# Performance work log

Measured on AMD Instinct MI355X. Metric: run time of the kernel, lower is better.

The kernel has to match this reference:

```python
import jax, jax.numpy as jnp
import numpy as np


def setup_inputs() -> dict:
    key = jax.random.key(0)
    k1, k2, k3 = jax.random.split(key, 3)
    B, H, S, D = 2, 16, 2048, 128
    q = jax.random.normal(k1, (B, H, S, D), dtype=jnp.float32)
    k = jax.random.normal(k2, (B, H, S, D), dtype=jnp.float32)
    v = jax.random.normal(k3, (B, H, S, D), dtype=jnp.float32)
    mask = jnp.ones((1, 1, S, S), dtype=bool)  # broadcastable; mask==0 -> -inf
    scale = jnp.array(1.0, dtype=jnp.float32)  # learnable scalar nn.Parameter
    return {"q": q, "k": k, "v": v, "mask": mask, "scale": scale}


def reference(q, k, v, mask, scale):
    # scores = (q @ k^T) * scale  -> [B,H,S,S]
    scores = jnp.einsum("bhsd,bhtd->bhst", q, k) * scale
    scores = jnp.where(mask, scores, -jnp.inf)
    attn = jax.nn.softmax(scores, axis=-1)
    out = jnp.einsum("bhst,bhtd->bhsd", attn, v)
    return out
```

## Files before the change

### kernel.cpp

```cpp
#include <hip/hip_runtime.h>
#include <hip/hip_bf16.h>
#include <math.h>
#include <stdint.h>

#define Bn 2
#define Hn 16
#define Sn 2048
#define Dn 128
#define KVBLK 64
#define NITER (Sn / KVBLK)
#define QBLK_WG 128
#define QT (Sn / QBLK_WG)
#define NWG (Bn * Hn * QT)
#define LOG2E 1.44269504088896340736f
#define RESCALE_THR 8.0f

typedef _Float16 f16x8 __attribute__((ext_vector_type(8)));
typedef _Float16 f16x4 __attribute__((ext_vector_type(4)));
typedef float f32x16 __attribute__((ext_vector_type(16)));
typedef int i32x4 __attribute__((ext_vector_type(4)));

__device__ __forceinline__ void swap32(int& a, int& b) {
    asm("v_permlane32_swap_b32 %0, %1" : "+v"(a), "+v"(b));
}

__global__ __launch_bounds__(256, 2)
void attn_fwd(const float* __restrict__ qp, const float* __restrict__ kp,
              const float* __restrict__ vp, const float* __restrict__ scale_p,
              float* __restrict__ op) {
    __shared__ _Float16 lds_k[KVBLK * Dn];
    __shared__ _Float16 lds_vt[Dn * KVBLK];

    const int tid  = threadIdx.x;
    const int wave = tid >> 6;
    const int lane = tid & 63;
    const int l31  = lane & 31;
    const int h    = lane >> 5;

    const int bid = blockIdx.x;
    const int wg  = (bid & 7) * (NWG / 8) + (bid >> 3);
    const int bh  = wg / QT;
    const int qt  = wg % QT;
    const int q0w = qt * QBLK_WG + wave * 32;

    const float lam = scale_p[0] * LOG2E;
    const size_t base = (size_t)bh * Sn * Dn;
    const float* qg = qp + base;
    const float* kg = kp + base;
    const float* vg = vp + base;

    f16x8 qf[8];
    {
        const float* qrow = qg + (size_t)(q0w + l31) * Dn + h * 8;
#pragma unroll
        for (int c = 0; c < 8; ++c) {
            float4 x = *(const float4*)(qrow + c * 16);
            float4 y = *(const float4*)(qrow + c * 16 + 4);
            f16x8 t;
            t[0] = (_Float16)(x.x * lam); t[1] = (_Float16)(x.y * lam);
            t[2] = (_Float16)(x.z * lam); t[3] = (_Float16)(x.w * lam);
            t[4] = (_Float16)(y.x * lam); t[5] = (_Float16)(y.y * lam);
            t[6] = (_Float16)(y.z * lam); t[7] = (_Float16)(y.w * lam);
            qf[c] = t;
        }
    }

    float4 kreg[8];
    float  vreg[32];
    const int vd  = tid & 127;
    const int vkb = (tid >> 7) * 32;

    auto load_tiles = [&](int it) {
        const int kv0 = it * KVBLK;
#pragma unroll
        for (int p = 0; p < 8; ++p) {
            const int idx = p * 256 + tid;
            kreg[p] = *(const float4*)(kg + (size_t)(kv0 + (idx >> 5)) * Dn + ((idx & 31) << 2));
        }
        const float* col = vg + (size_t)(kv0 + vkb) * Dn + vd;
#pragma unroll
        for (int j = 0; j < 32; ++j) vreg[j] = col[(size_t)j * Dn];
    };

    auto store_tiles = [&]() {
#pragma unroll
        for (int p = 0; p < 8; ++p) {
            const int idx = p * 256 + tid;
            const int kv = idx >> 5, d4 = (idx & 31) << 2;
            f16x4 w = { (_Float16)kreg[p].x, (_Float16)kreg[p].y,
                        (_Float16)kreg[p].z, (_Float16)kreg[p].w };
            const int byte = (kv * 256 + d4 * 2) ^ ((kv & 15) << 4);
            *(f16x4*)((char*)lds_k + byte) = w;
        }
#pragma unroll
        for (int w8 = 0; w8 < 4; ++w8) {
            f16x8 t;
#pragma unroll
            for (int e = 0; e < 8; ++e) t[e] = (_Float16)vreg[8 * w8 + e];
            const int byte = (vd * 128 + (vkb + 8 * w8) * 2) ^ ((vd & 7) << 4);
            *(f16x8*)((char*)lds_vt + byte) = t;
        }
    };

    f32x16 acc[4];
#pragma unroll
    for (int dt = 0; dt < 4; ++dt)
#pragma unroll
        for (int r = 0; r < 16; ++r) acc[dt][r] = 0.f;
    float m_run = -INFINITY, l_run = 0.f;

    const int swzk = (l31 & 15) << 4;
    const int swzv = (l31 & 7) << 4;

    load_tiles(0);
    for (int it = 0; it < NITER; ++it) {
        __syncthreads();
        store_tiles();
        __syncthreads();
        if (it + 1 < NITER) load_tiles(it + 1);

        f32x16 st[2];
#pragma unroll
        for (int s = 0; s < 2; ++s)
#pragma unroll
            for (int r = 0; r < 16; ++r) st[s][r] = 0.f;
#pragma unroll
        for (int s = 0; s < 2; ++s) {
            const char* kbase = (const char*)lds_k + (32 * s + l31) * 256;
#pragma unroll
            for (int c = 0; c < 8; ++c) {
                f16x8 kf = *(const f16x8*)(kbase + ((c * 32 + h * 16) ^ swzk));
                st[s] = __builtin_amdgcn_mfma_f32_32x32x16_f16(kf, qf[c], st[s], 0, 0, 0);
            }
        }

        float pmax = st[0][0];
#pragma unroll
        for (int r = 1; r < 16; ++r) pmax = fmaxf(pmax, st[0][r]);
#pragma unroll
        for (int r = 0; r < 16; ++r) pmax = fmaxf(pmax, st[1][r]);
        const float rowmax = fmaxf(pmax, __shfl_xor(pmax, 32, 64));

        if (!__all(rowmax <= m_run + RESCALE_THR)) {
            const float mnew = fmaxf(m_run, rowmax);
            const float corr = exp2f(m_run - mnew);
            m_run = mnew;
            l_run *= corr;
#pragma unroll
            for (int dt = 0; dt < 4; ++dt)
#pragma unroll
                for (int r = 0; r < 16; ++r) acc[dt][r] *= corr;
        }

        float rs = 0.f;
#pragma unroll
        for (int s = 0; s < 2; ++s)
#pragma unroll
            for (int r = 0; r < 16; ++r) {
                const float pv = exp2f(st[s][r] - m_run);
                st[s][r] = pv;
                rs += pv;
            }
        l_run += rs + __shfl_xor(rs, 32, 64);

        int pk[2][4][2];
#pragma unroll
        for (int s = 0; s < 2; ++s)
#pragma unroll
            for (int c4 = 0; c4 < 4; ++c4) {
                pk[s][c4][0] = __builtin_bit_cast(int,
                    __builtin_amdgcn_cvt_pkrtz(st[s][4 * c4 + 0], st[s][4 * c4 + 1]));
                pk[s][c4][1] = __builtin_bit_cast(int,
                    __builtin_amdgcn_cvt_pkrtz(st[s][4 * c4 + 2], st[s][4 * c4 + 3]));
            }

#pragma unroll
        for (int ks = 0; ks < 4; ++ks) {
            const int s = ks >> 1, c0 = (ks & 1) * 2;
            int a0 = pk[s][c0][0],     a1 = pk[s][c0][1];
            int b0 = pk[s][c0 + 1][0], b1 = pk[s][c0 + 1][1];
            swap32(a0, b0);
            swap32(a1, b1);
            i32x4 bi = { a0, a1, b0, b1 };
            f16x8 bf = __builtin_bit_cast(f16x8, bi);
            const int voff = (ks * 32 + h * 16) ^ swzv;
#pragma unroll
            for (int dt = 0; dt < 4; ++dt) {
                f16x8 vf = *(const f16x8*)((const char*)lds_vt + (32 * dt + l31) * 128 + voff);
                acc[dt] = __builtin_amdgcn_mfma_f32_32x32x16_f16(vf, bf, acc[dt], 0, 0, 0);
            }
        }
    }

    const float inv = 1.0f / l_run;
    float* orow = op + base + (size_t)(q0w + l31) * Dn;
#pragma unroll
    for (int dt = 0; dt < 4; ++dt)
#pragma unroll
        for (int rg = 0; rg < 4; ++rg) {
            float4 w = { acc[dt][4 * rg + 0] * inv, acc[dt][4 * rg + 1] * inv,
                         acc[dt][4 * rg + 2] * inv, acc[dt][4 * rg + 3] * inv };
            *(float4*)(orow + 32 * dt + 8 * rg + 4 * h) = w;
        }
}

extern "C" void kernel_launch(void* const* d_in, const int* in_sizes, int n_in,
                              void* d_out, int out_size, void* d_ws, size_t ws_size,
                              hipStream_t stream) {
    const float* q = (const float*)d_in[0];
    const float* k = (const float*)d_in[1];
    const float* v = (const float*)d_in[2];
    const float* scale = (const float*)d_in[4];
    float* out = (float*)d_out;
    attn_fwd<<<dim3(NWG), dim3(256), 0, stream>>>(q, k, v, scale, out);
}
```

Measured before the change: 115.0 us.

## Pre-convert K/V to swizzled fp16 tiles and pipeline attention with async LDS loads

Adds a prep kernel that converts K and V to fp16 and writes them in pre-swizzled, transposed tile layout into workspace. The main kernel, now with 8 waves of 16 query rows using 16x16x32 MFMAs, streams these tiles into double-buffered LDS with global_load_lds. It software-pipelines QK^T of one tile with PV of the previous one, passing P through LDS. It also uses the hardware exp2 builtin and raises wave priority around the MFMA blocks. This trades an extra kernel launch and workspace traffic for halved K/V bytes in the hot loop and overlapped loads, with a fallback path if the workspace is too small.

```diff
diff --git a/kernel.cpp b/kernel.cpp
--- a/kernel.cpp
+++ b/kernel.cpp
@@ -14,20 +14,258 @@
 #define NWG (Bn * Hn * QT)
 #define LOG2E 1.44269504088896340736f
 #define RESCALE_THR 8.0f
+#define TILE_BYTES 16384
+#define NTILES (Bn * Hn * NITER)
+#define WS_NEEDED ((size_t)2 * NTILES * TILE_BYTES)
 
 typedef _Float16 f16x8 __attribute__((ext_vector_type(8)));
 typedef _Float16 f16x4 __attribute__((ext_vector_type(4)));
+typedef float f32x4 __attribute__((ext_vector_type(4)));
 typedef float f32x16 __attribute__((ext_vector_type(16)));
 typedef int i32x4 __attribute__((ext_vector_type(4)));
 
+#define EXP2F(x) __builtin_amdgcn_exp2f(x)
+
 __device__ __forceinline__ void swap32(int& a, int& b) {
     asm("v_permlane32_swap_b32 %0, %1" : "+v"(a), "+v"(b));
 }
 
+__device__ __forceinline__ void gload16(const char* g, char* l) {
+    __builtin_amdgcn_global_load_lds(
+        (const __attribute__((address_space(1))) void*)g,
+        (__attribute__((address_space(3))) void*)(uint32_t)(uintptr_t)l,
+        16, 0, 0);
+}
+
+__global__ __launch_bounds__(256)
+void prep_kv(const float* __restrict__ kp, const float* __restrict__ vp,
+             char* __restrict__ wsk, char* __restrict__ wsv) {
+    const int blk = blockIdx.x;
+    const int bh = blk / NITER, t = blk % NITER;
+    const int tid = threadIdx.x;
+    const size_t gbase = (size_t)bh * Sn * Dn + (size_t)t * KVBLK * Dn;
+    const float* kg = kp + gbase;
+    const float* vg = vp + gbase;
+    char* ok = wsk + (size_t)blk * TILE_BYTES;
+    char* ov = wsv + (size_t)blk * TILE_BYTES;
+
+#pragma unroll
+    for (int p = 0; p < 8; ++p) {
+        const int idx = p * 256 + tid;
+        const int kv = idx >> 5, d4 = (idx & 31) << 2;
+        float4 x = *(const float4*)(kg + kv * Dn + d4);
+        f16x4 w = { (_Float16)x.x, (_Float16)x.y, (_Float16)x.z, (_Float16)x.w };
+        *(f16x4*)(ok + ((kv * 256 + d4 * 2) ^ ((kv & 15) << 4))) = w;
+    }
+    const int vd = tid & 127, vkb = (tid >> 7) * 32;
+    const float* col = vg + vkb * Dn + vd;
+    float vr[32];
+#pragma unroll
+    for (int j = 0; j < 32; ++j) vr[j] = col[j * Dn];
+#pragma unroll
+    for (int w8 = 0; w8 < 4; ++w8) {
+        f16x8 tt;
+#pragma unroll
+        for (int e = 0; e < 8; ++e) tt[e] = (_Float16)vr[8 * w8 + e];
+        *(f16x8*)(ov + ((vd * 128 + (vkb + 8 * w8) * 2) ^ ((vd & 7) << 4))) = tt;
+    }
+}
+
+__global__ __launch_bounds__(512, 4)
+void attn_fwd_opt(const float* __restrict__ qp, const char* __restrict__ wsk,
+                  const char* __restrict__ wsv, const float* __restrict__ scale_p,
+                  float* __restrict__ op) {
+    __shared__ _Float16 lds_k[2][KVBLK * Dn];
+    __shared__ _Float16 lds_v[2][Dn * KVBLK];
+    __shared__ char     lds_p[8][2048];
+
+    const int tid  = threadIdx.x;
+    const int wave = tid >> 6;
+    const int lane = tid & 63;
+    const int r16  = lane & 15;
+    const int g    = lane >> 4;
+
+    const int bid = blockIdx.x;
+    const int wg  = (bid & 7) * (NWG / 8) + (bid >> 3);
+    const int bh  = wg / QT;
+    const int qt  = wg % QT;
+    const int q0w = qt * QBLK_WG + wave * 16;
+
+    const float lam = scale_p[0] * LOG2E;
+    const size_t base = (size_t)bh * Sn * Dn;
+
+    f16x8 qf[4];
+    {
+        const float* qrow = qp + base + (size_t)(q0w + r16) * Dn + g * 8;
+#pragma unroll
+        for (int c = 0; c < 4; ++c) {
+            float4 x = *(const float4*)(qrow + c * 32);
+            float4 y = *(const float4*)(qrow + c * 32 + 4);
+            f16x8 t;
+            t[0] = (_Float16)(x.x * lam); t[1] = (_Float16)(x.y * lam);
+            t[2] = (_Float16)(x.z * lam); t[3] = (_Float16)(x.w * lam);
+            t[4] = (_Float16)(y.x * lam); t[5] = (_Float16)(y.y * lam);
+            t[6] = (_Float16)(y.z * lam); t[7] = (_Float16)(y.w * lam);
+            qf[c] = t;
+        }
+    }
+
+    const int swzk = r16 << 4;
+    const int swzv = (r16 & 7) << 4;
+    int koff[4], voff[2], pw[4], pr[2];
+#pragma unroll
+    for (int c = 0; c < 4; ++c) koff[c] = r16 * 256 + ((c * 64 + g * 16) ^ swzk);
+#pragma unroll
+    for (int kc = 0; kc < 2; ++kc) voff[kc] = r16 * 128 + ((kc * 64 + g * 16) ^ swzv);
+#pragma unroll
+    for (int kt = 0; kt < 4; ++kt) pw[kt] = wave * 2048 + (r16 * 128 + ((kt * 32 + g * 8) ^ swzv));
+#pragma unroll
+    for (int kc = 0; kc < 2; ++kc) pr[kc] = wave * 2048 + (r16 * 128 + ((kc * 64 + g * 16) ^ swzv));
+    char* pldsb = (char*)&lds_p[0][0];
+
+    const char* wk = wsk + (size_t)bh * NITER * TILE_BYTES;
+    const char* wv = wsv + (size_t)bh * NITER * TILE_BYTES;
+    const int seg = wave * 1024 + lane * 16;
+
+    f32x4 zv4 = {0.f, 0.f, 0.f, 0.f};
+    f32x4 acc[8];
+#pragma unroll
+    for (int dt = 0; dt < 8; ++dt) acc[dt] = zv4;
+    float m_run = -INFINITY, l_run = 0.f;
+
+    {
+        const char* sk = wk + seg;
+        char* dk = (char*)&lds_k[0][0] + seg;
+        gload16(sk, dk); gload16(sk + 8192, dk + 8192);
+    }
+
+#define BODY(T, P, DO_PV, STAGE_K)                                             \
+    {                                                                          \
+        asm volatile("s_waitcnt vmcnt(0)" ::: "memory");                       \
+        __builtin_amdgcn_s_barrier();                                          \
+        if (STAGE_K) {                   \
+            const char* sk = wk + (size_t)(T + 1) * TILE_BYTES + seg;          \
+            char* dk = (char*)&lds_k[(P) ^ 1][0] + seg;                        \
+            gload16(sk, dk); gload16(sk + 8192, dk + 8192);                    \
+        }                                                                      \
+        {                                    \
+            const char* sv = wv + (size_t)(T) * TILE_BYTES + seg;              \
+            char* dv = (char*)&lds_v[P][0] + seg;                              \
+            gload16(sv, dv); gload16(sv + 8192, dv + 8192);                    \
+        }                                                                      \
+        const char* kbp = (const char*)&lds_k[P][0];                           \
+        f32x4 st[4];                                                           \
+        __builtin_amdgcn_s_setprio(1);                                         \
+        _Pragma("unroll")                                                      \
+        for (int kt = 0; kt < 4; ++kt) {                                       \
+            f16x8 kf = *(const f16x8*)(kbp + kt * 4096 + koff[0]);             \
+            st[kt] = __builtin_amdgcn_mfma_f32_16x16x32_f16(kf, qf[0], zv4, 0, 0, 0); \
+        }                                                                      \
+        _Pragma("unroll")                                                      \
+        for (int c = 1; c < 4; ++c)                                            \
+            _Pragma("unroll")                                                  \
+            for (int kt = 0; kt < 4; ++kt) {                                   \
+                f16x8 kf = *(const f16x8*)(kbp + kt * 4096 + koff[c]);         \
+                st[kt] = __builtin_amdgcn_mfma_f32_16x16x32_f16(kf, qf[c], st[kt], 0, 0, 0); \
+            }                                                                  \
+        if (DO_PV) {  \
+            const char* vbp = (const char*)&lds_v[(P) ^ 1][0];                 \
+            f16x8 pb0 = *(const f16x8*)(pldsb + pr[0]);                        \
+            f16x8 pb1 = *(const f16x8*)(pldsb + pr[1]);                        \
+            _Pragma("unroll")                                                  \
+            for (int dt = 0; dt < 8; ++dt) {                                   \
+                f16x8 v0 = *(const f16x8*)(vbp + dt * 2048 + voff[0]);         \
+                f16x8 v1 = *(const f16x8*)(vbp + dt * 2048 + voff[1]);         \
+                acc[dt] = __builtin_amdgcn_mfma_f32_16x16x32_f16(v0, pb0, acc[dt], 0, 0, 0); \
+                acc[dt] = __builtin_amdgcn_mfma_f32_16x16x32_f16(v1, pb1, acc[dt], 0, 0, 0); \
+            }                                                                  \
+        }                                                                      \
+        __builtin_amdgcn_s_setprio(0);                                         \
+                               \
+        float mx[8];                                                           \
+        _Pragma("unroll")                                                      \
+        for (int i = 0; i < 8; ++i)                                            \
+            mx[i] = fmaxf(st[i >> 1][(i & 1) * 2], st[i >> 1][(i & 1) * 2 + 1]); \
+        _Pragma("unroll")                                                      \
+        for (int off = 4; off >= 1; off >>= 1)                                 \
+            _Pragma("unroll")                                                  \
+            for (int i = 0; i < off; ++i) mx[i] = fmaxf(mx[i], mx[i + off]);   \
+        float rowmax = fmaxf(mx[0], __shfl_xor(mx[0], 16, 64));                \
+        rowmax = fmaxf(rowmax, __shfl_xor(rowmax, 32, 64));                    \
+        if (!__all(rowmax <= m_run + RESCALE_THR)) {        \
+            const float mnew = fmaxf(m_run, rowmax);                           \
+            const float corr = EXP2F(m_run - mnew);                            \
+            m_run = mnew;                                                      \
+            l_run *= corr;                                                     \
+            _Pragma("unroll")                                                  \
+            for (int dt = 0; dt < 8; ++dt)                                     \
+                _Pragma("unroll")                                              \
+                for (int j = 0; j < 4; ++j) acc[dt][j] *= corr;                \
+        }                                                                      \
+        float s0 = 0.f, s1 = 0.f;                                              \
+        _Pragma("unroll")                                                      \
+        for (int kt = 0; kt < 4; ++kt)                                         \
+            _Pragma("unroll")                                                  \
+            for (int j = 0; j < 4; ++j) {                                      \
+                const float pv = EXP2F(st[kt][j] - m_run);                     \
+                st[kt][j] = pv;                                                \
+                if (j & 1) s1 += pv; else s0 += pv;                            \
+            }                                                                  \
+        float rs = s0 + s1;                                                    \
+        rs += __shfl_xor(rs, 16, 64);                                          \
+        rs += __shfl_xor(rs, 32, 64);                                          \
+        l_run += rs;                                                           \
+                        \
+        _Pragma("unroll")                                                      \
+        for (int kt = 0; kt < 4; ++kt) {                                       \
+            uint32_t w0 = __builtin_bit_cast(uint32_t,                         \
+                __builtin_amdgcn_cvt_pkrtz(st[kt][0], st[kt][1]));             \
+            uint32_t w1 = __builtin_bit_cast(uint32_t,                         \
+                __builtin_amdgcn_cvt_pkrtz(st[kt][2], st[kt][3]));             \
+            uint2 ww = { w0, w1 };                                             \
+            *(uint2*)(pldsb + pw[kt]) = ww;                                    \
+        }                                                                      \
+    }
+
+    BODY(0, 0, false, true)
+    for (int tp = 1; tp + 1 < NITER; tp += 2) {
+        BODY(tp,     1, true, true)
+        BODY(tp + 1, 0, true, true)
+    }
+    BODY(NITER - 1, 1, true, false)
+
+    asm volatile("s_waitcnt vmcnt(0)" ::: "memory");
+    __builtin_amdgcn_s_barrier();
+    {
+        const char* vbp = (const char*)&lds_v[1][0];
+        f16x8 pb0 = *(const f16x8*)(pldsb + pr[0]);
+        f16x8 pb1 = *(const f16x8*)(pldsb + pr[1]);
+        __builtin_amdgcn_s_setprio(1);
+#pragma unroll
+        for (int dt = 0; dt < 8; ++dt) {
+            f16x8 v0 = *(const f16x8*)(vbp + dt * 2048 + voff[0]);
+            f16x8 v1 = *(const f16x8*)(vbp + dt * 2048 + voff[1]);
+            acc[dt] = __builtin_amdgcn_mfma_f32_16x16x32_f16(v0, pb0, acc[dt], 0, 0, 0);
+            acc[dt] = __builtin_amdgcn_mfma_f32_16x16x32_f16(v1, pb1, acc[dt], 0, 0, 0);
+        }
+        __builtin_amdgcn_s_setprio(0);
+    }
+
+    const float inv = 1.0f / l_run;
+    float* orow = op + base + (size_t)(q0w + r16) * Dn;
+#pragma unroll
+    for (int dt = 0; dt < 8; ++dt) {
+        float4 w = { acc[dt][0] * inv, acc[dt][1] * inv,
+                     acc[dt][2] * inv, acc[dt][3] * inv };
+        *(float4*)(orow + dt * 16 + g * 4) = w;
+    }
+#undef BODY
+}
+
 __global__ __launch_bounds__(256, 2)
-void attn_fwd(const float* __restrict__ qp, const float* __restrict__ kp,
-              const float* __restrict__ vp, const float* __restrict__ scale_p,
-              float* __restrict__ op) {
+void attn_fwd_fb(const float* __restrict__ qp, const float* __restrict__ kp,
+                 const float* __restrict__ vp, const float* __restrict__ scale_p,
+                 float* __restrict__ op) {
     __shared__ _Float16 lds_k[KVBLK * Dn];
     __shared__ _Float16 lds_vt[Dn * KVBLK];
 
@@ -49,6 +287,7 @@
     const float* kg = kp + base;
     const float* vg = vp + base;
 
+    typedef f32x16 accv;
     f16x8 qf[8];
     {
         const float* qrow = qg + (size_t)(q0w + l31) * Dn + h * 8;
@@ -102,7 +341,7 @@
         }
     };
 
-    f32x16 acc[4];
+    accv acc[4];
 #pragma unroll
     for (int dt = 0; dt < 4; ++dt)
 #pragma unroll
@@ -119,7 +358,7 @@
         __syncthreads();
         if (it + 1 < NITER) load_tiles(it + 1);
 
-        f32x16 st[2];
+        accv st[2];
 #pragma unroll
         for (int s = 0; s < 2; ++s)
 #pragma unroll
@@ -143,7 +382,7 @@
 
         if (!__all(rowmax <= m_run + RESCALE_THR)) {
             const float mnew = fmaxf(m_run, rowmax);
-            const float corr = exp2f(m_run - mnew);
+            const float corr = EXP2F(m_run - mnew);
             m_run = mnew;
             l_run *= corr;
 #pragma unroll
@@ -157,7 +396,7 @@
         for (int s = 0; s < 2; ++s)
 #pragma unroll
             for (int r = 0; r < 16; ++r) {
-                const float pv = exp2f(st[s][r] - m_run);
+                const float pv = EXP2F(st[s][r] - m_run);
                 st[s][r] = pv;
                 rs += pv;
             }
@@ -212,5 +451,13 @@
     const float* v = (const float*)d_in[2];
     const float* scale = (const float*)d_in[4];
     float* out = (float*)d_out;
-    attn_fwd<<<dim3(NWG), dim3(256), 0, stream>>>(q, k, v, scale, out);
-}
+
+    if (ws_size >= WS_NEEDED) {
+        char* wsk = (char*)d_ws;
+        char* wsv = wsk + (size_t)NTILES * TILE_BYTES;
+        prep_kv<<<dim3(NTILES), dim3(256), 0, stream>>>(k, v, wsk, wsv);
+        attn_fwd_opt<<<dim3(NWG), dim3(512), 0, stream>>>(q, wsk, wsv, scale, out);
+    } else {
+        attn_fwd_fb<<<dim3(NWG), dim3(256), 0, stream>>>(q, k, v, scale, out);
+    }
+}
```

After: 102.5 us. 10.8% less time.
